# Kernel tuning notes

Measured on AMD Instinct MI355X. Metric: run time of the kernel, lower is better.

The kernel has to match this reference:

```python
import jax, jax.numpy as jnp
import numpy as np

S, N, K = 8, 2048, 64          # snapshots, atoms, max neighbors (sum of max_num_neighs)
L = 20.0                        # periodic box length
R_CS, R_C = 6.0, 12.0           # smooth cutoff radii
M2 = 16                         # dim_sub_net


def _mlp(x, params, resnet=False):
    # DenseChainNet: Linear -> relu per layer; resnet skip when dims match or double (DeepMD style)
    for W, b in params:
        y = jax.nn.relu(x @ W + b)
        if resnet and y.shape[-1] == x.shape[-1]:
            y = y + x
        elif resnet and y.shape[-1] == 2 * x.shape[-1]:
            y = y + jnp.concatenate([x, x], axis=-1)
        x = y
    return x


def setup_inputs() -> dict:
    ks = jax.random.split(jax.random.key(0), 14)
    inputs = jax.random.uniform(ks[0], (S, N, 3), jnp.float32) * L
    input_types = jax.random.randint(ks[1], (S, N), 0, 2)
    nl = jax.random.randint(ks[2], (S, N, K), 0, N)
    neigh_list = jnp.where(jax.random.uniform(ks[3], (S, N, K)) < 0.2, -1, nl)  # -1 = padded neighbor

    def w(k, i, o):
        return jax.random.normal(k, (i, o), jnp.float32) / np.float32(np.sqrt(i))

    return {
        'inputs': inputs,
        'input_types': input_types,
        'neigh_list': neigh_list,
        'length': jnp.array([L, L, L], jnp.float32),
        # embed_species (species_dim [2,16,32])
        'ew0': w(ks[4], 2, 16), 'eb0': jnp.zeros((16,), jnp.float32),
        'ew1': w(ks[5], 16, 32), 'eb1': jnp.zeros((32,), jnp.float32),
        # fit_species (species_fit [32,32,31])
        'fw0': w(ks[6], 32, 32), 'fb0': jnp.zeros((32,), jnp.float32),
        'fw1': w(ks[7], 32, 31), 'fb1': jnp.zeros((31,), jnp.float32),
        # embed_net (descript_dim [32,64,128], resnet=True)
        'gw0': w(ks[8], 32, 64), 'gb0': jnp.zeros((64,), jnp.float32),
        'gw1': w(ks[9], 64, 128), 'gb1': jnp.zeros((128,), jnp.float32),
    }


def reference(inputs, input_types, neigh_list, length,
              ew0, eb0, ew1, eb1, fw0, fb0, fw1, fb1, gw0, gb0, gw1, gb1):
    mask = neigh_list == -1                                   # [S,N,K]
    idx = jnp.where(mask, 0, neigh_list)

    # ---- gen_coordinates_smooth: neighbor gather + min-image + smooth cutoff ----
    neigh_pos = jax.vmap(lambda p, i: p[i])(inputs, idx)      # [S,N,K,3]
    diff = neigh_pos - inputs[:, :, None, :]
    diff = diff - length * jnp.round(diff / length)           # minimum image convention
    rsq = jnp.sum(diff * diff, axis=-1)
    r = jnp.sqrt(jnp.where(rsq > 0, rsq, 1.0))                # safe sqrt (self/padded pairs)
    inv = 1.0 / r
    u = (r - R_CS) / (R_C - R_CS)
    sw = jnp.where(r < R_CS, inv,
                   jnp.where(r < R_C, inv * (0.5 * jnp.cos(jnp.pi * u) + 0.5), 0.0))
    valid = (~mask) & (rsq > 0)
    s_ij = jnp.where(valid, sw, 0.0)                          # [S,N,K]  s(r)
    r_ij = diff * (s_ij / r)[..., None]                       # [S,N,K,3] s(r)*x/r

    # ---- SpeciesModule: pair-type embedding (symmetrized) ----
    neigh_types = jax.vmap(lambda t, i: t[i])(input_types, idx)           # [S,N,K]
    center = jnp.broadcast_to(input_types[:, :, None], (S, N, K))
    pairs = jnp.stack([center, neigh_types], axis=-1).astype(jnp.float32).reshape(-1, 2)
    emb = [(ew0, eb0), (ew1, eb1)]
    t = _mlp(pairs, emb) + _mlp(pairs[:, ::-1], emb)
    td = _mlp(t, [(fw0, fb0), (fw1, fb1)]).reshape(S, N, K, -1)           # [S,N,K,31]
    td = jnp.where(mask[..., None], 0.0, td)

    # ---- embedding net + descriptor contraction ----
    s_tilde = jnp.concatenate([td, s_ij[..., None]], axis=-1)             # [S,N,K,32]
    G = _mlp(s_tilde.reshape(S * N * K, -1), [(gw0, gb0), (gw1, gb1)],
             resnet=True).reshape(S, N, K, -1)                            # [S,N,K,128]
    r_tilde = jnp.concatenate([s_ij[..., None], r_ij], axis=-1)           # [S,N,K,4]
    G2 = G[..., :M2]
    R = jnp.einsum('snkd,snkm->sndm', r_tilde, G2)                        # [S,N,4,16]
    R1 = jnp.einsum('snkd,sndm->snkm', r_tilde, R)                        # [S,N,K,16]
    D = jnp.einsum('snke,snkm->snem', G, R1)                              # [S,N,128,16]
    return D
```

## Files before the change

### kernel.cpp

```cpp
#include <hip/hip_runtime.h>
#include <math.h>

#define S_DIM 8
#define N_DIM 2048
#define K_DIM 64
#define APW 4
#define ST_ST 40
#define ST_H1 72

typedef __attribute__((ext_vector_type(8))) short bf16x8;
typedef __attribute__((ext_vector_type(4))) float f32x4;
typedef __attribute__((ext_vector_type(4))) int   i32x4;

__device__ __forceinline__ unsigned asu(float x) {
    union { float f; unsigned u; } v; v.f = x; return v.u;
}
__device__ __forceinline__ unsigned short f2bf(float x) {
    unsigned u = asu(x);
    return (unsigned short)((u + 0x7FFFu + ((u >> 16) & 1u)) >> 16);
}
__device__ __forceinline__ float bf2f(unsigned short h) {
    union { unsigned u; float f; } v; v.u = ((unsigned)h) << 16; return v.f;
}
__device__ __forceinline__ unsigned rne_pk(float x, float y) {
    unsigned ux = asu(x), uy = asu(y);
    return ((ux + 0x7FFFu + ((ux >> 16) & 1u)) >> 16) |
           ((uy + 0x7FFFu + ((uy >> 16) & 1u)) & 0xFFFF0000u);
}
__device__ __forceinline__ unsigned trn_pk(float x, float y) {
    return (asu(x) >> 16) | (asu(y) & 0xFFFF0000u);
}
__device__ __forceinline__ bf16x8 half_frag(unsigned p0, unsigned p1) {
    union { i32x4 i; bf16x8 b; } u;
    u.i = (i32x4){(int)p0, (int)p1, 0, 0};
    return u.b;
}

__global__ __launch_bounds__(256) void prep_kernel(
        const float* __restrict__ ew0, const float* __restrict__ eb0,
        const float* __restrict__ ew1, const float* __restrict__ eb1,
        const float* __restrict__ fw0, const float* __restrict__ fb0,
        const float* __restrict__ fw1, const float* __restrict__ fb1,
        const float* __restrict__ gw0, const float* __restrict__ gw1,
        unsigned* __restrict__ td_pk,
        unsigned short* __restrict__ w0t, unsigned short* __restrict__ w1t) {
    __shared__ float l_ew0[32], l_eb0[16], l_ew1[512], l_eb1[32];
    __shared__ float l_fw0[1024], l_fb0[32], l_fw1[992], l_fb1[31];
    __shared__ float l_h[4][2][16];
    __shared__ float l_tv[4][32];
    __shared__ float l_f1[4][32];
    __shared__ float l_td[4][32];

    const int tid = threadIdx.x;
    if (tid < 32) l_ew0[tid] = ew0[tid];
    if (tid < 16) l_eb0[tid] = eb0[tid];
    for (int i = tid; i < 512; i += 256) l_ew1[i] = ew1[i];
    if (tid < 32) l_eb1[tid] = eb1[tid];
    for (int i = tid; i < 1024; i += 256) l_fw0[i] = fw0[i];
    if (tid < 32) l_fb0[tid] = fb0[tid];
    for (int i = tid; i < 992; i += 256) l_fw1[i] = fw1[i];
    if (tid < 31) l_fb1[tid] = fb1[tid];
    __syncthreads();

    if (tid < 128) {
        const int p = tid >> 5, ord = (tid >> 4) & 1, j = tid & 15;
        const float c = (float)(p >> 1), t = (float)(p & 1);
        const float x0 = ord ? t : c;
        const float x1 = ord ? c : t;
        l_h[p][ord][j] = fmaxf(x0 * l_ew0[j] + x1 * l_ew0[16 + j] + l_eb0[j], 0.f);
    }
    __syncthreads();
    if (tid < 128) {
        const int p = tid >> 5, j = tid & 31;
        float acc = 0.f;
#pragma unroll
        for (int ord = 0; ord < 2; ord++) {
            float v = l_eb1[j];
#pragma unroll
            for (int i = 0; i < 16; i++) v += l_h[p][ord][i] * l_ew1[i * 32 + j];
            acc += fmaxf(v, 0.f);
        }
        l_tv[p][j] = acc;
    }
    __syncthreads();
    if (tid < 128) {
        const int p = tid >> 5, j = tid & 31;
        float v = l_fb0[j];
#pragma unroll
        for (int i = 0; i < 32; i++) v += l_tv[p][i] * l_fw0[i * 32 + j];
        l_f1[p][j] = fmaxf(v, 0.f);
    }
    __syncthreads();
    if (tid < 128) {
        const int p = tid >> 5, j = tid & 31;
        if (j < 31) {
            float v = l_fb1[j];
#pragma unroll
            for (int i = 0; i < 32; i++) v += l_f1[p][i] * l_fw1[i * 31 + j];
            l_td[p][j] = fmaxf(v, 0.f);
        } else {
            l_td[p][31] = 0.f;
        }
    }
    __syncthreads();
    if (tid < 64) {
        const int p = tid >> 4, i = tid & 15;
        const unsigned lo = f2bf(l_td[p][2 * i]);
        const unsigned hi = (i == 15) ? 0u : (unsigned)f2bf(l_td[p][2 * i + 1]);
        td_pk[tid] = lo | (hi << 16);
    }

    for (int idx = tid; idx < 2048; idx += 256) {
        const int j = idx >> 5, i = idx & 31;
        w0t[idx] = f2bf(gw0[i * 64 + j]);
    }
    for (int idx = tid; idx < 8192; idx += 256) {
        const int e = idx >> 6, j = idx & 63;
        w1t[idx] = f2bf(gw1[j * 128 + e]);
    }
}

__global__ __launch_bounds__(64, 2) void descr_mfma(
    const float* __restrict__ inputs, const int* __restrict__ input_types,
    const int* __restrict__ neigh_list, const float* __restrict__ length,
    const float* __restrict__ gb0, const float* __restrict__ gb1,
    const unsigned* __restrict__ td_pk, const unsigned short* __restrict__ w0t,
    const unsigned short* __restrict__ w1t, float* __restrict__ out)
{
    __shared__ __align__(16) unsigned short s_st[64 * ST_ST];
    __shared__ __align__(16) unsigned short s_h1[64 * ST_H1];
    __shared__ __align__(16) float s_rtT[4 * 68];
    __shared__ unsigned s_tdpk[64];
    float* s_A = (float*)s_st;

    const int lane = threadIdx.x;
    const int l15 = lane & 15;
    const int q = lane >> 4;

    bf16x8 w0f[4];
#pragma unroll
    for (int nt = 0; nt < 4; nt++)
        w0f[nt] = *(const bf16x8*)&w0t[(nt * 16 + l15) * 32 + q * 8];
    bf16x8 w1f[8][2];
#pragma unroll
    for (int et = 0; et < 8; et++) {
        w1f[et][0] = *(const bf16x8*)&w1t[(et * 16 + l15) * 64 + q * 8];
        w1f[et][1] = *(const bf16x8*)&w1t[(et * 16 + l15) * 64 + 32 + q * 8];
    }
    float b0f[4], b1f[8];
#pragma unroll
    for (int jt = 0; jt < 4; jt++) b0f[jt] = gb0[jt * 16 + l15];
#pragma unroll
    for (int et = 0; et < 8; et++) b1f[et] = gb1[et * 16 + l15];
    s_tdpk[lane] = td_pk[lane];
    const float Lx = length[0], Ly = length[1], Lz = length[2];
    const float iLx = 1.f / Lx, iLy = 1.f / Ly, iLz = 1.f / Lz;

    const f32x4 zf = {0.f, 0.f, 0.f, 0.f};

    for (int aa = 0; aa < APW; aa++) {
        const int atom = blockIdx.x * APW + aa;
        const int sidx = atom >> 11;

        __syncthreads();

        {
            const int nb = neigh_list[atom * K_DIM + lane];
            const bool msk = nb < 0;
            const int idx = msk ? 0 : nb;
            const float cx = inputs[atom * 3 + 0];
            const float cy = inputs[atom * 3 + 1];
            const float cz = inputs[atom * 3 + 2];
            const int nbase = (sidx * N_DIM + idx) * 3;
            float dx = inputs[nbase + 0] - cx;
            float dy = inputs[nbase + 1] - cy;
            float dz = inputs[nbase + 2] - cz;
            dx -= Lx * rintf(dx * iLx);
            dy -= Ly * rintf(dy * iLy);
            dz -= Lz * rintf(dz * iLz);
            const float rsq = dx * dx + dy * dy + dz * dz;
            const float r = sqrtf(rsq > 0.f ? rsq : 1.f);
            const float inv = 1.f / r;
            float sw;
            if (r < 6.f) sw = inv;
            else if (r < 12.f) {
                const float u = (r - 6.f) * (1.f / 6.f);
                sw = inv * (0.5f * __cosf(3.14159265358979323846f * u) + 0.5f);
            } else sw = 0.f;
            const bool valid = (!msk) && (rsq > 0.f);
            const float sij = valid ? sw : 0.f;
            const float f = sij * inv;
            s_rtT[0 * 68 + lane] = sij;
            s_rtT[1 * 68 + lane] = dx * f;
            s_rtT[2 * 68 + lane] = dy * f;
            s_rtT[3 * 68 + lane] = dz * f;

            const int ct = input_types[atom];
            const int ntp = input_types[sidx * N_DIM + idx];
            const unsigned* tdr = &s_tdpk[(ct * 2 + ntp) * 16];
            const unsigned zmask = msk ? 0u : 0xFFFFFFFFu;
            unsigned* strow = (unsigned*)&s_st[lane * ST_ST];
#pragma unroll
            for (int i = 0; i < 15; i++) strow[i] = tdr[i] & zmask;
            strow[15] = (tdr[15] & zmask & 0xFFFFu) | (((unsigned)f2bf(sij)) << 16);
            strow[16] = 0; strow[17] = 0; strow[18] = 0; strow[19] = 0;
        }
        __syncthreads();

        bf16x8 rtf[4];
#pragma unroll
        for (int a = 0; a < 4; a++) {
            const f32x4 rv = *(const f32x4*)&s_rtT[(l15 & 3) * 68 + a * 16 + q * 4];
            rtf[a] = half_frag(rne_pk(rv[0], rv[1]), rne_pk(rv[2], rv[3]));
        }

        f32x4 Bj[4] = {zf, zf, zf, zf};
#pragma unroll
        for (int mt = 0; mt < 4; mt++) {
            const bf16x8 afr = *(const bf16x8*)&s_st[(mt * 16 + l15) * ST_ST + q * 8];
            f32x4 c1[4];
#pragma unroll
            for (int jt = 0; jt < 4; jt++)
                c1[jt] = __builtin_amdgcn_mfma_f32_16x16x32_bf16(afr, w0f[jt], zf, 0, 0, 0);
#pragma unroll
            for (int jt = 0; jt < 4; jt++) {
                float hv[4];
#pragma unroll
                for (int reg = 0; reg < 4; reg++) {
                    const int k = mt * 16 + q * 4 + reg;
                    const float r = bf2f(s_st[k * ST_ST + (jt & 1) * 16 + l15]);
                    hv[reg] = fmaxf(c1[jt][reg] + b0f[jt], 0.f) + r;
                    s_h1[k * ST_H1 + jt * 16 + l15] = f2bf(hv[reg]);
                }
                const bf16x8 hf = half_frag(trn_pk(hv[0], hv[1]), trn_pk(hv[2], hv[3]));
                Bj[jt] = __builtin_amdgcn_mfma_f32_16x16x32_bf16(rtf[mt], hf, Bj[jt], 0, 0, 0);
            }
        }
        __syncthreads();

        f32x4 AT[8] = {zf, zf, zf, zf, zf, zf, zf, zf};
#pragma unroll
        for (int kt = 0; kt < 4; kt++) {
            const bf16x8 a0 = *(const bf16x8*)&s_h1[(kt * 16 + l15) * ST_H1 + q * 8];
            const bf16x8 a1 = *(const bf16x8*)&s_h1[(kt * 16 + l15) * ST_H1 + 32 + q * 8];
#pragma unroll
            for (int et = 0; et < 8; et++) {
                f32x4 c2 = __builtin_amdgcn_mfma_f32_16x16x32_bf16(a0, w1f[et][0], zf, 0, 0, 0);
                c2 = __builtin_amdgcn_mfma_f32_16x16x32_bf16(a1, w1f[et][1], c2, 0, 0, 0);
                const float g0 = fmaxf(c2[0] + b1f[et], 0.f);
                const float g1 = fmaxf(c2[1] + b1f[et], 0.f);
                const float g2 = fmaxf(c2[2] + b1f[et], 0.f);
                const float g3 = fmaxf(c2[3] + b1f[et], 0.f);
                const bf16x8 gf = half_frag(trn_pk(g0, g1), trn_pk(g2, g3));
                AT[et] = __builtin_amdgcn_mfma_f32_16x16x32_bf16(rtf[kt], gf, AT[et], 0, 0, 0);
            }
        }

        if (lane < 16) {
#pragma unroll
            for (int et = 0; et < 8; et++) {
                const f32x4 v = AT[et] + Bj[et & 3];
                *(f32x4*)&s_A[(et * 16 + lane) * 4] = v;
            }
        }
        __syncthreads();

        {
            const int m0 = (lane & 3) * 4;
            const int er = lane >> 2;
            f32x4 Am[4];
#pragma unroll
            for (int t = 0; t < 4; t++) Am[t] = *(const f32x4*)&s_A[(m0 + t) * 4];
            float* op = out + (size_t)atom * 2048;
#pragma unroll
            for (int g = 0; g < 8; g++) {
                const int e = g * 16 + er;
                const f32x4 Ae = *(const f32x4*)&s_A[e * 4];
                f32x4 o;
                o[0] = Ae[0]*Am[0][0] + Ae[1]*Am[0][1] + Ae[2]*Am[0][2] + Ae[3]*Am[0][3];
                o[1] = Ae[0]*Am[1][0] + Ae[1]*Am[1][1] + Ae[2]*Am[1][2] + Ae[3]*Am[1][3];
                o[2] = Ae[0]*Am[2][0] + Ae[1]*Am[2][1] + Ae[2]*Am[2][2] + Ae[3]*Am[2][3];
                o[3] = Ae[0]*Am[3][0] + Ae[1]*Am[3][1] + Ae[2]*Am[3][2] + Ae[3]*Am[3][3];
                *(f32x4*)&op[e * 16 + m0] = o;
            }
        }
    }
}

extern "C" void kernel_launch(void* const* d_in, const int* in_sizes, int n_in,
                              void* d_out, int out_size, void* d_ws, size_t ws_size,
                              hipStream_t stream) {
    (void)in_sizes; (void)n_in; (void)out_size; (void)ws_size;
    const float* inputs      = (const float*)d_in[0];
    const int*   input_types = (const int*)d_in[1];
    const int*   neigh_list  = (const int*)d_in[2];
    const float* length      = (const float*)d_in[3];
    const float* ew0 = (const float*)d_in[4];
    const float* eb0 = (const float*)d_in[5];
    const float* ew1 = (const float*)d_in[6];
    const float* eb1 = (const float*)d_in[7];
    const float* fw0 = (const float*)d_in[8];
    const float* fb0 = (const float*)d_in[9];
    const float* fw1 = (const float*)d_in[10];
    const float* fb1 = (const float*)d_in[11];
    const float* gw0 = (const float*)d_in[12];
    const float* gb0 = (const float*)d_in[13];
    const float* gw1 = (const float*)d_in[14];
    const float* gb1 = (const float*)d_in[15];
    float* out = (float*)d_out;

    unsigned* td_pk = (unsigned*)d_ws;
    unsigned short* w0t = (unsigned short*)((char*)d_ws + 512);
    unsigned short* w1t = (unsigned short*)((char*)d_ws + 512 + 4096);

    hipLaunchKernelGGL(prep_kernel, dim3(1), dim3(256), 0, stream,
                       ew0, eb0, ew1, eb1, fw0, fb0, fw1, fb1, gw0, gw1,
                       td_pk, w0t, w1t);

    const int nblocks = (S_DIM * N_DIM) / APW;
    hipLaunchKernelGGL(descr_mfma, dim3(nblocks), dim3(64), 0, stream,
                       inputs, input_types, neigh_list, length,
                       gb0, gb1, td_pk, w0t, w1t, out);
}
```

Before: 229.3 us.

## Keep MLP hidden activations in registers via transposed MFMA and identity-matrix shuffles

The first embedding layer is computed transposed (weights as A operand, features as B), so its outputs land in registers laid out for direct reuse as the A fragment of the second layer. This removes the s_h1 and s_st shared-memory staging and one barrier per atom. The resnet skip terms are produced with MFMAs against identity fragments instead of LDS reads, and the r_tilde values are stored as bf16. In exchange the kernel issues extra MFMA work for the identity products and keeps more values live in registers, which may raise register pressure.

```diff
diff --git a/kernel.cpp b/kernel.cpp
--- a/kernel.cpp
+++ b/kernel.cpp
@@ -5,8 +5,6 @@
 #define N_DIM 2048
 #define K_DIM 64
 #define APW 4
-#define ST_ST 40
-#define ST_H1 72
 
 typedef __attribute__((ext_vector_type(8))) short bf16x8;
 typedef __attribute__((ext_vector_type(4))) float f32x4;
@@ -18,9 +16,6 @@
 __device__ __forceinline__ unsigned short f2bf(float x) {
     unsigned u = asu(x);
     return (unsigned short)((u + 0x7FFFu + ((u >> 16) & 1u)) >> 16);
-}
-__device__ __forceinline__ float bf2f(unsigned short h) {
-    union { unsigned u; float f; } v; v.u = ((unsigned)h) << 16; return v.f;
 }
 __device__ __forceinline__ unsigned rne_pk(float x, float y) {
     unsigned ux = asu(x), uy = asu(y);
@@ -30,10 +25,9 @@
 __device__ __forceinline__ unsigned trn_pk(float x, float y) {
     return (asu(x) >> 16) | (asu(y) & 0xFFFF0000u);
 }
-__device__ __forceinline__ bf16x8 half_frag(unsigned p0, unsigned p1) {
-    union { i32x4 i; bf16x8 b; } u;
-    u.i = (i32x4){(int)p0, (int)p1, 0, 0};
-    return u.b;
+union F8 { i32x4 i; bf16x8 b; };
+__device__ __forceinline__ bf16x8 mkfrag(unsigned a, unsigned b, unsigned c, unsigned d) {
+    F8 u; u.i = (i32x4){(int)a, (int)b, (int)c, (int)d}; return u.b;
 }
 
 __global__ __launch_bounds__(256) void prep_kernel(
@@ -109,7 +103,6 @@
         const unsigned hi = (i == 15) ? 0u : (unsigned)f2bf(l_td[p][2 * i + 1]);
         td_pk[tid] = lo | (hi << 16);
     }
-
     for (int idx = tid; idx < 2048; idx += 256) {
         const int j = idx >> 5, i = idx & 31;
         w0t[idx] = f2bf(gw0[i * 64 + j]);
@@ -127,35 +120,61 @@
     const unsigned* __restrict__ td_pk, const unsigned short* __restrict__ w0t,
     const unsigned short* __restrict__ w1t, float* __restrict__ out)
 {
-    __shared__ __align__(16) unsigned short s_st[64 * ST_ST];
-    __shared__ __align__(16) unsigned short s_h1[64 * ST_H1];
-    __shared__ __align__(16) float s_rtT[4 * 68];
-    __shared__ unsigned s_tdpk[64];
-    float* s_A = (float*)s_st;
+    __shared__ __align__(16) unsigned short s_rtb[4 * 68];
+    __shared__ __align__(16) unsigned s_tdpk[80];
+    __shared__ int s_sel[64];
+    __shared__ __align__(16) float s_A[128 * 4];
 
     const int lane = threadIdx.x;
-    const int l15 = lane & 15;
+    const int l = lane & 15;
     const int q = lane >> 4;
 
     bf16x8 w0f[4];
 #pragma unroll
-    for (int nt = 0; nt < 4; nt++)
-        w0f[nt] = *(const bf16x8*)&w0t[(nt * 16 + l15) * 32 + q * 8];
-    bf16x8 w1f[8][2];
-#pragma unroll
-    for (int et = 0; et < 8; et++) {
-        w1f[et][0] = *(const bf16x8*)&w1t[(et * 16 + l15) * 64 + q * 8];
-        w1f[et][1] = *(const bf16x8*)&w1t[(et * 16 + l15) * 64 + 32 + q * 8];
-    }
-    float b0f[4], b1f[8];
-#pragma unroll
-    for (int jt = 0; jt < 4; jt++) b0f[jt] = gb0[jt * 16 + l15];
-#pragma unroll
-    for (int et = 0; et < 8; et++) b1f[et] = gb1[et * 16 + l15];
+    for (int jt = 0; jt < 4; jt++)
+        w0f[jt] = *(const bf16x8*)&w0t[(jt * 16 + l) * 32 + q * 8];
+
+    bf16x8 w1p[8][2];
+#pragma unroll
+    for (int et = 0; et < 8; et++)
+#pragma unroll
+        for (int P = 0; P < 2; P++) {
+            const uint2 a = *(const uint2*)&w1t[(et * 16 + l) * 64 + (2 * P) * 16 + q * 4];
+            const uint2 b = *(const uint2*)&w1t[(et * 16 + l) * 64 + (2 * P + 1) * 16 + q * 4];
+            w1p[et][P] = mkfrag(a.x, a.y, b.x, b.y);
+        }
+
+    bf16x8 idAf[2];
+#pragma unroll
+    for (int p = 0; p < 2; p++) {
+        unsigned d[4];
+#pragma unroll
+        for (int t = 0; t < 4; t++) {
+            const unsigned lo = (q * 8 + 2 * t == p * 16 + l) ? 0x3F80u : 0u;
+            const unsigned hi = (q * 8 + 2 * t + 1 == p * 16 + l) ? 0x3F800000u : 0u;
+            d[t] = lo | hi;
+        }
+        idAf[p] = mkfrag(d[0], d[1], d[2], d[3]);
+    }
+    unsigned ed0, ed1;
+    {
+        ed0 = ((q * 4 + 0 == l) ? 0x3F80u : 0u) | ((q * 4 + 1 == l) ? 0x3F800000u : 0u);
+        ed1 = ((q * 4 + 2 == l) ? 0x3F80u : 0u) | ((q * 4 + 3 == l) ? 0x3F800000u : 0u);
+    }
+    const bf16x8 ef_even = mkfrag(ed0, ed1, 0, 0);
+    const bf16x8 ef_odd  = mkfrag(0, 0, ed0, ed1);
+
+    f32x4 b0v[4];
+#pragma unroll
+    for (int jt = 0; jt < 4; jt++) b0v[jt] = *(const f32x4*)&gb0[jt * 16 + q * 4];
+    float b1f[8];
+#pragma unroll
+    for (int et = 0; et < 8; et++) b1f[et] = gb1[et * 16 + l];
+
     s_tdpk[lane] = td_pk[lane];
+    if (lane < 16) s_tdpk[64 + lane] = 0u;
     const float Lx = length[0], Ly = length[1], Lz = length[2];
     const float iLx = 1.f / Lx, iLy = 1.f / Ly, iLz = 1.f / Lz;
-
     const f32x4 zf = {0.f, 0.f, 0.f, 0.f};
 
     for (int aa = 0; aa < APW; aa++) {
@@ -190,78 +209,75 @@
             const bool valid = (!msk) && (rsq > 0.f);
             const float sij = valid ? sw : 0.f;
             const float f = sij * inv;
-            s_rtT[0 * 68 + lane] = sij;
-            s_rtT[1 * 68 + lane] = dx * f;
-            s_rtT[2 * 68 + lane] = dy * f;
-            s_rtT[3 * 68 + lane] = dz * f;
-
+            s_rtb[0 * 68 + lane] = f2bf(sij);
+            s_rtb[1 * 68 + lane] = f2bf(dx * f);
+            s_rtb[2 * 68 + lane] = f2bf(dy * f);
+            s_rtb[3 * 68 + lane] = f2bf(dz * f);
             const int ct = input_types[atom];
             const int ntp = input_types[sidx * N_DIM + idx];
-            const unsigned* tdr = &s_tdpk[(ct * 2 + ntp) * 16];
-            const unsigned zmask = msk ? 0u : 0xFFFFFFFFu;
-            unsigned* strow = (unsigned*)&s_st[lane * ST_ST];
-#pragma unroll
-            for (int i = 0; i < 15; i++) strow[i] = tdr[i] & zmask;
-            strow[15] = (tdr[15] & zmask & 0xFFFFu) | (((unsigned)f2bf(sij)) << 16);
-            strow[16] = 0; strow[17] = 0; strow[18] = 0; strow[19] = 0;
+            s_sel[lane] = msk ? 4 : (ct * 2 + ntp);
         }
         __syncthreads();
 
-        bf16x8 rtf[4];
-#pragma unroll
-        for (int a = 0; a < 4; a++) {
-            const f32x4 rv = *(const f32x4*)&s_rtT[(l15 & 3) * 68 + a * 16 + q * 4];
-            rtf[a] = half_frag(rne_pk(rv[0], rv[1]), rne_pk(rv[2], rv[3]));
-        }
-
-        f32x4 Bj[4] = {zf, zf, zf, zf};
+        bf16x8 stf[4];
 #pragma unroll
         for (int mt = 0; mt < 4; mt++) {
-            const bf16x8 afr = *(const bf16x8*)&s_st[(mt * 16 + l15) * ST_ST + q * 8];
-            f32x4 c1[4];
-#pragma unroll
-            for (int jt = 0; jt < 4; jt++)
-                c1[jt] = __builtin_amdgcn_mfma_f32_16x16x32_bf16(afr, w0f[jt], zf, 0, 0, 0);
+            const int sel = s_sel[mt * 16 + l];
+            i32x4 v = *(const i32x4*)&s_tdpk[sel * 16 + q * 4];
+            const unsigned sij16 = (unsigned)s_rtb[0 * 68 + mt * 16 + l];
+            const int w3 = (q == 3) ? (int)(((unsigned)v.w & 0xFFFFu) | (sij16 << 16)) : v.w;
+            F8 u; u.i = (i32x4){v.x, v.y, v.z, w3};
+            stf[mt] = u.b;
+        }
+
+        uint2 hpk[4][4];
+#pragma unroll
+        for (int mt = 0; mt < 4; mt++) {
+            const f32x4 res0 = __builtin_amdgcn_mfma_f32_16x16x32_bf16(idAf[0], stf[mt], zf, 0, 0, 0);
+            const f32x4 res1 = __builtin_amdgcn_mfma_f32_16x16x32_bf16(idAf[1], stf[mt], zf, 0, 0, 0);
 #pragma unroll
             for (int jt = 0; jt < 4; jt++) {
-                float hv[4];
-#pragma unroll
-                for (int reg = 0; reg < 4; reg++) {
-                    const int k = mt * 16 + q * 4 + reg;
-                    const float r = bf2f(s_st[k * ST_ST + (jt & 1) * 16 + l15]);
-                    hv[reg] = fmaxf(c1[jt][reg] + b0f[jt], 0.f) + r;
-                    s_h1[k * ST_H1 + jt * 16 + l15] = f2bf(hv[reg]);
-                }
-                const bf16x8 hf = half_frag(trn_pk(hv[0], hv[1]), trn_pk(hv[2], hv[3]));
-                Bj[jt] = __builtin_amdgcn_mfma_f32_16x16x32_bf16(rtf[mt], hf, Bj[jt], 0, 0, 0);
+                const f32x4 c1 = __builtin_amdgcn_mfma_f32_16x16x32_bf16(w0f[jt], stf[mt], b0v[jt], 0, 0, 0);
+                const f32x4& rr = (jt & 1) ? res1 : res0;
+                const float h0 = fmaxf(c1[0], 0.f) + rr[0];
+                const float h1 = fmaxf(c1[1], 0.f) + rr[1];
+                const float h2 = fmaxf(c1[2], 0.f) + rr[2];
+                const float h3 = fmaxf(c1[3], 0.f) + rr[3];
+                hpk[jt][mt].x = rne_pk(h0, h1);
+                hpk[jt][mt].y = rne_pk(h2, h3);
             }
         }
-        __syncthreads();
 
         f32x4 AT[8] = {zf, zf, zf, zf, zf, zf, zf, zf};
 #pragma unroll
         for (int kt = 0; kt < 4; kt++) {
-            const bf16x8 a0 = *(const bf16x8*)&s_h1[(kt * 16 + l15) * ST_H1 + q * 8];
-            const bf16x8 a1 = *(const bf16x8*)&s_h1[(kt * 16 + l15) * ST_H1 + 32 + q * 8];
+            const bf16x8 af0 = mkfrag(hpk[0][kt].x, hpk[0][kt].y, hpk[1][kt].x, hpk[1][kt].y);
+            const bf16x8 af1 = mkfrag(hpk[2][kt].x, hpk[2][kt].y, hpk[3][kt].x, hpk[3][kt].y);
+            const uint2 rv = *(const uint2*)&s_rtb[(l & 3) * 68 + kt * 16 + q * 4];
+            const bf16x8 rtf = mkfrag(rv.x, rv.y, 0, 0);
+            f32x4 Q[4];
+            Q[0] = __builtin_amdgcn_mfma_f32_16x16x32_bf16(af0, ef_even, zf, 0, 0, 0);
+            Q[1] = __builtin_amdgcn_mfma_f32_16x16x32_bf16(af0, ef_odd,  zf, 0, 0, 0);
+            Q[2] = __builtin_amdgcn_mfma_f32_16x16x32_bf16(af1, ef_even, zf, 0, 0, 0);
+            Q[3] = __builtin_amdgcn_mfma_f32_16x16x32_bf16(af1, ef_odd,  zf, 0, 0, 0);
 #pragma unroll
             for (int et = 0; et < 8; et++) {
-                f32x4 c2 = __builtin_amdgcn_mfma_f32_16x16x32_bf16(a0, w1f[et][0], zf, 0, 0, 0);
-                c2 = __builtin_amdgcn_mfma_f32_16x16x32_bf16(a1, w1f[et][1], c2, 0, 0, 0);
-                const float g0 = fmaxf(c2[0] + b1f[et], 0.f);
-                const float g1 = fmaxf(c2[1] + b1f[et], 0.f);
-                const float g2 = fmaxf(c2[2] + b1f[et], 0.f);
-                const float g3 = fmaxf(c2[3] + b1f[et], 0.f);
-                const bf16x8 gf = half_frag(trn_pk(g0, g1), trn_pk(g2, g3));
-                AT[et] = __builtin_amdgcn_mfma_f32_16x16x32_bf16(rtf[kt], gf, AT[et], 0, 0, 0);
+                f32x4 c2 = __builtin_amdgcn_mfma_f32_16x16x32_bf16(af0, w1p[et][0], zf, 0, 0, 0);
+                c2 = __builtin_amdgcn_mfma_f32_16x16x32_bf16(af1, w1p[et][1], c2, 0, 0, 0);
+                const f32x4& qq = Q[et & 3];
+                const float g0 = fmaxf(c2[0] + b1f[et], 0.f) + qq[0];
+                const float g1 = fmaxf(c2[1] + b1f[et], 0.f) + qq[1];
+                const float g2 = fmaxf(c2[2] + b1f[et], 0.f) + qq[2];
+                const float g3 = fmaxf(c2[3] + b1f[et], 0.f) + qq[3];
+                const bf16x8 gp = mkfrag(trn_pk(g0, g1), trn_pk(g2, g3), 0, 0);
+                AT[et] = __builtin_amdgcn_mfma_f32_16x16x32_bf16(rtf, gp, AT[et], 0, 0, 0);
             }
         }
 
         if (lane < 16) {
 #pragma unroll
-            for (int et = 0; et < 8; et++) {
-                const f32x4 v = AT[et] + Bj[et & 3];
-                *(f32x4*)&s_A[(et * 16 + lane) * 4] = v;
-            }
+            for (int et = 0; et < 8; et++)
+                *(f32x4*)&s_A[(et * 16 + lane) * 4] = AT[et];
         }
         __syncthreads();
 
```

Measured after the change: 233.6 us. No clear change (+1.9%).
